# Optimization experiments

Hardware: AMD Instinct MI355X
Metric: run time of the kernel (lower is better)

Reference implementation:

```python
import jax, jax.numpy as jnp
import numpy as np
import math


def setup_inputs() -> dict:
    key = jax.random.key(0)
    k_fm, k_x, k_y, k_w, k_h = jax.random.split(key, 5)
    C, H, W = 512, 256, 256
    N = 4096
    patch_num = 4
    pe = 2  # sqrt(patch_num)
    feature_map = jax.random.normal(k_fm, (C, H, W), dtype=jnp.float32)
    # Boxes fully inside the map with per-patch extent >= 2 so every sub-box is valid.
    min_wh = 2.0 * pe + 1.0
    x0 = jax.random.uniform(k_x, (N,), minval=0.0, maxval=W / 2 - 1.0)
    y0 = jax.random.uniform(k_y, (N,), minval=0.0, maxval=H / 2 - 1.0)
    w = jax.random.uniform(k_w, (N,), minval=min_wh, maxval=W / 2 - 2.0)
    h = jax.random.uniform(k_h, (N,), minval=min_wh, maxval=H / 2 - 2.0)
    roi_batch = jnp.stack([x0, y0, x0 + w, y0 + h], axis=1).astype(jnp.float32)
    return {"feature_map": feature_map, "roi_batch": roi_batch, "patch_num": patch_num}


def _box_indices(roi_batch, patch_num, W):
    """Rounded, clamped per-patch sub-box corners; shapes (P, N), flattened patch-major."""
    pe = int(math.isqrt(patch_num))
    xmin, ymin, xmax, ymax = (roi_batch[:, k] for k in range(4))
    i = jnp.arange(patch_num)
    ix = (i % pe).astype(roi_batch.dtype)[:, None]
    iy = (i // pe).astype(roi_batch.dtype)[:, None]
    ws = ((xmax - xmin) / pe)[None, :]
    hs = ((ymax - ymin) / pe)[None, :]
    ax = xmin[None, :] + ix * ws  # (P, N)
    ay = ymin[None, :] + iy * hs
    clampi = lambda v: jnp.clip(jnp.round(v), 0, W - 1).astype(jnp.int32)
    x0, x1 = clampi(ax), clampi(ax + ws)
    y0, y1 = clampi(ay), clampi(ay + hs)
    flat = lambda a: a.reshape(-1)  # loop order: patch outer, roi inner
    return flat(x0), flat(x1), flat(y0), flat(y1)


def reference(feature_map, roi_batch, patch_num):
    C, H, W = feature_map.shape
    x0, x1, y0, y1 = _box_indices(roi_batch, patch_num, W)
    cw = x1 - x0
    ch = y1 - y0
    mask = (cw >= 1) & (ch >= 1)  # (P*N,)
    # Integral image with zero row/col padding: S[:, y, x] = sum of fm[:, :y, :x]
    S = jnp.pad(jnp.cumsum(jnp.cumsum(feature_map, axis=1), axis=2),
                ((0, 0), (1, 0), (1, 0)))
    # Region sums via 4-corner gather: (C, B)
    sums = S[:, y1, x1] - S[:, y0, x1] - S[:, y1, x0] + S[:, y0, x0]
    area = jnp.maximum(cw * ch, 1).astype(feature_map.dtype)
    pooled = (sums / area).T  # (B, C) region means == adaptive_avg_pool2d(.,(1,1))
    pooled = pooled * mask.astype(feature_map.dtype)[:, None]
    return pooled[:, :, None, None], mask.astype(jnp.int32)
```

## Files before the change

kernel.cpp:

```cpp
#include <hip/hip_runtime.h>


#define CHN 512
#define HD  256
#define WD  256
#define SP  257
#define YC  8
#define NK  32
#define OP_OFF 33817088UL

#define BAR() do { asm volatile("s_waitcnt lgkmcnt(0)" ::: "memory"); \
                   __builtin_amdgcn_s_barrier(); \
                   asm volatile("" ::: "memory"); } while (0)

__global__ __launch_bounds__(512, 4) void fusedScanK(const float* __restrict__ fm,
                                                     float* __restrict__ S) {
    __shared__ float tile[2][32][260];
    const int t = threadIdx.x, lane = t & 63, w = t >> 6;
    const int c0 = blockIdx.x * 32;
    const int k  = blockIdx.y;
    const int y0 = k * YC;

    const int cg = t & 7;
    const int x8 = t >> 3;
    const float4 z4 = make_float4(0.f, 0.f, 0.f, 0.f);

    if (k == 0) {
        #pragma unroll
        for (int it = 0; it < 4; ++it) {
            const int lin = it * 512 + t;
            const int cgg = lin & 7, x = lin >> 3;
            *(float4*)(S + (size_t)x * CHN + c0 + 4 * cgg) = z4;
        }
    }

    float4 cur[4], nxt[4];
    #pragma unroll
    for (int j = 0; j < 4; ++j)
        cur[j] = *(const float4*)(fm + ((size_t)(c0 + w * 4 + j) << 16)
                                     + (size_t)y0 * 256 + 4 * lane);

    float4 acc[4];
    #pragma unroll
    for (int m = 0; m < 4; ++m) acc[m] = z4;

    const int wcol = (4 * lane) ^ (4 * w);
    const int rxor = 4 * cg;

    for (int y = 0; y < YC; ++y) {
        const int buf = y & 1;
        if (y < YC - 1) {
            #pragma unroll
            for (int j = 0; j < 4; ++j)
                nxt[j] = *(const float4*)(fm + ((size_t)(c0 + w * 4 + j) << 16)
                                             + (size_t)(y0 + y + 1) * 256 + 4 * lane);
        }
        #pragma unroll
        for (int j = 0; j < 4; ++j) {
            const float4 v = cur[j];
            const float local = ((v.x + v.y) + v.z) + v.w;
            float s = local;
            #pragma unroll
            for (int d = 1; d < 64; d <<= 1) {
                float u = __shfl_up(s, d, 64);
                if (lane >= d) s += u;
            }
            const float e = s - local;
            float4 p;
            p.x = e   + v.x;
            p.y = p.x + v.y;
            p.z = p.y + v.z;
            p.w = p.z + v.w;
            *(float4*)&tile[buf][w * 4 + j][wcol] = p;
        }
        BAR();
        const size_t rowb = ((size_t)(y0 + y + 1) * SP) * CHN;
        #pragma unroll
        for (int m = 0; m < 4; ++m) {
            const int x = x8 + 64 * m;
            const int xs = x ^ rxor;
            float4 a = acc[m];
            a.x += tile[buf][4 * cg + 0][xs];
            a.y += tile[buf][4 * cg + 1][xs];
            a.z += tile[buf][4 * cg + 2][xs];
            a.w += tile[buf][4 * cg + 3][xs];
            acc[m] = a;
            *(float4*)(S + rowb + (size_t)(x + 1) * CHN + c0 + 4 * cg) = a;
        }
        if (t < 8)
            *(float4*)(S + rowb + c0 + 4 * t) = z4;
        #pragma unroll
        for (int j = 0; j < 4; ++j) cur[j] = nxt[j];
    }
}

__global__ __launch_bounds__(256) void offsetK(const float* __restrict__ S,
                                               float* __restrict__ OP) {
    const int gid = blockIdx.x * 256 + threadIdx.x;
    const int c = gid & 511, x = gid >> 9;
    OP[((size_t)0 * SP + x) * CHN + c] = 0.0f;
    OP[((size_t)1 * SP + x) * CHN + c] = 0.0f;
    double run = 0.0;
    #pragma unroll
    for (int j = 0; j < NK - 1; ++j) {
        run += (double)S[((size_t)(YC * (j + 1)) * SP + x) * CHN + c];
        OP[((size_t)(j + 2) * SP + x) * CHN + c] = (float)run;
    }
}

__global__ __launch_bounds__(256) void gatherK(const float* __restrict__ S,
                                              const float* __restrict__ OP,
                                              const float* __restrict__ roi,
                                              float* __restrict__ out,
                                              float* __restrict__ maskOut,
                                              int N) {
    const int n = blockIdx.x;
    const float xmin = roi[4 * n + 0];
    const float ymin = roi[4 * n + 1];
    const float xmax = roi[4 * n + 2];
    const float ymax = roi[4 * n + 3];

    const float wsv = __fdiv_rn(__fsub_rn(xmax, xmin), 2.0f);
    const float hsv = __fdiv_rn(__fsub_rn(ymax, ymin), 2.0f);
    const float ax1 = __fadd_rn(xmin, wsv);
    const float ay1 = __fadd_rn(ymin, hsv);
    const float lim = (float)(WD - 1);

    int rx[3], ry[3];
    rx[0] = (int)fminf(fmaxf(rintf(xmin), 0.0f), lim);
    rx[1] = (int)fminf(fmaxf(rintf(ax1), 0.0f), lim);
    rx[2] = (int)fminf(fmaxf(rintf(__fadd_rn(ax1, wsv)), 0.0f), lim);
    ry[0] = (int)fminf(fmaxf(rintf(ymin), 0.0f), lim);
    ry[1] = (int)fminf(fmaxf(rintf(ay1), 0.0f), lim);
    ry[2] = (int)fminf(fmaxf(rintf(__fadd_rn(ay1, hsv)), 0.0f), lim);

    const int t = threadIdx.x;
    float2 g[3][3];
    #pragma unroll
    for (int j = 0; j < 3; ++j) {
        const int kk = (ry[j] + YC - 1) >> 3;
        #pragma unroll
        for (int i = 0; i < 3; ++i) {
            const float2 l = *(const float2*)(S  + ((size_t)ry[j] * SP + rx[i]) * CHN + 2 * t);
            const float2 o = *(const float2*)(OP + ((size_t)kk   * SP + rx[i]) * CHN + 2 * t);
            g[j][i] = make_float2(l.x + o.x, l.y + o.y);
        }
    }

    float m[4];
    #pragma unroll
    for (int p = 0; p < 4; ++p) {
        const int ix = p & 1, iy = p >> 1;
        const int cw = rx[ix + 1] - rx[ix];
        const int ch = ry[iy + 1] - ry[iy];
        const int maskv = (cw >= 1 && ch >= 1) ? 1 : 0;
        int areai = cw * ch; if (areai < 1) areai = 1;
        const float areaf = (float)areai;
        const float maskf = (float)maskv;
        m[p] = maskf;

        const float2 s11 = g[iy + 1][ix + 1];
        const float2 s01 = g[iy][ix + 1];
        const float2 s10 = g[iy + 1][ix];
        const float2 s00 = g[iy][ix];
        float2 o;
        o.x = __fdiv_rn(((s11.x - s01.x) - s10.x) + s00.x, areaf) * maskf;
        o.y = __fdiv_rn(((s11.y - s01.y) - s10.y) + s00.y, areaf) * maskf;
        *(float2*)(out + ((size_t)p * N + n) * CHN + 2 * t) = o;
    }
    if (t < 4) maskOut[(size_t)t * N + n] = m[t];
}

extern "C" void kernel_launch(void* const* d_in, const int* in_sizes, int n_in,
                              void* d_out, int out_size, void* d_ws, size_t ws_size,
                              hipStream_t stream) {
    const float* fm  = (const float*)d_in[0];
    const float* roi = (const float*)d_in[1];

    const int N = in_sizes[1] / 4;
    const int B = 4 * N;

    float* S  = (float*)d_ws;
    float* OP = (float*)d_ws + OP_OFF;
    float* out     = (float*)d_out;
    float* maskOut = out + (size_t)B * CHN;

    dim3 gF(CHN / 32, NK);
    fusedScanK<<<gF, 512, 0, stream>>>(fm, S);

    offsetK<<<(SP * CHN) / 256, 256, 0, stream>>>(S, OP);

    gatherK<<<N, 256, 0, stream>>>(S, OP, roi, out, maskOut, N);
}
```

Baseline: 266.8 us.

## Re-layout integral image into channel-block-major tiles of 32 channels

Changes the summed-area table and the per-block offset table from a [y][x][512-channel] layout to [channel-block][y][x][32], and updates all three kernels to match. Each scan block now writes one contiguous region per row instead of 128-byte pieces spread with a 2 KB stride, which should improve write locality. The cost is that each gather block now reads 16 separate 128-byte segments at far-apart addresses per corner, instead of one contiguous 2 KB span. The offset kernel also has to use a div/mod to recover its indices.

```diff
diff --git a/kernel.cpp b/kernel.cpp
--- a/kernel.cpp
+++ b/kernel.cpp
@@ -9,6 +9,9 @@
 #define NK  32
 #define OP_OFF 33817088UL
 
+#define SIDX(cb, y, x)  ((((size_t)(cb) * SP + (y)) * SP + (x)) * 32)
+#define OPIDX(cb, kk, x) ((((size_t)(cb) * 33 + (kk)) * SP + (x)) * 32)
+
 #define BAR() do { asm volatile("s_waitcnt lgkmcnt(0)" ::: "memory"); \
                    __builtin_amdgcn_s_barrier(); \
                    asm volatile("" ::: "memory"); } while (0)
@@ -17,7 +20,8 @@
                                                      float* __restrict__ S) {
     __shared__ float tile[2][32][260];
     const int t = threadIdx.x, lane = t & 63, w = t >> 6;
-    const int c0 = blockIdx.x * 32;
+    const int cb = blockIdx.x;
+    const int c0 = cb * 32;
     const int k  = blockIdx.y;
     const int y0 = k * YC;
 
@@ -30,7 +34,7 @@
         for (int it = 0; it < 4; ++it) {
             const int lin = it * 512 + t;
             const int cgg = lin & 7, x = lin >> 3;
-            *(float4*)(S + (size_t)x * CHN + c0 + 4 * cgg) = z4;
+            *(float4*)(S + SIDX(cb, 0, x) + 4 * cgg) = z4;
         }
     }
 
@@ -74,7 +78,7 @@
             *(float4*)&tile[buf][w * 4 + j][wcol] = p;
         }
         BAR();
-        const size_t rowb = ((size_t)(y0 + y + 1) * SP) * CHN;
+        const size_t rowb = SIDX(cb, y0 + y + 1, 0);
         #pragma unroll
         for (int m = 0; m < 4; ++m) {
             const int x = x8 + 64 * m;
@@ -85,10 +89,10 @@
             a.z += tile[buf][4 * cg + 2][xs];
             a.w += tile[buf][4 * cg + 3][xs];
             acc[m] = a;
-            *(float4*)(S + rowb + (size_t)(x + 1) * CHN + c0 + 4 * cg) = a;
+            *(float4*)(S + rowb + (size_t)(x + 1) * 32 + 4 * cg) = a;
         }
         if (t < 8)
-            *(float4*)(S + rowb + c0 + 4 * t) = z4;
+            *(float4*)(S + rowb + 4 * t) = z4;
         #pragma unroll
         for (int j = 0; j < 4; ++j) cur[j] = nxt[j];
     }
@@ -97,14 +101,17 @@
 __global__ __launch_bounds__(256) void offsetK(const float* __restrict__ S,
                                                float* __restrict__ OP) {
     const int gid = blockIdx.x * 256 + threadIdx.x;
-    const int c = gid & 511, x = gid >> 9;
-    OP[((size_t)0 * SP + x) * CHN + c] = 0.0f;
-    OP[((size_t)1 * SP + x) * CHN + c] = 0.0f;
+    const int cc = gid & 31;
+    const int xr = gid >> 5;
+    const int x  = xr % SP;
+    const int cb = xr / SP;
+    OP[OPIDX(cb, 0, x) + cc] = 0.0f;
+    OP[OPIDX(cb, 1, x) + cc] = 0.0f;
     double run = 0.0;
     #pragma unroll
     for (int j = 0; j < NK - 1; ++j) {
-        run += (double)S[((size_t)(YC * (j + 1)) * SP + x) * CHN + c];
-        OP[((size_t)(j + 2) * SP + x) * CHN + c] = (float)run;
+        run += (double)S[SIDX(cb, YC * (j + 1), x) + cc];
+        OP[OPIDX(cb, j + 2, x) + cc] = (float)run;
     }
 }
 
@@ -135,14 +142,16 @@
     ry[2] = (int)fminf(fmaxf(rintf(__fadd_rn(ay1, hsv)), 0.0f), lim);
 
     const int t = threadIdx.x;
+    const int cbb = t >> 4;
+    const int cc  = (t & 15) * 2;
     float2 g[3][3];
     #pragma unroll
     for (int j = 0; j < 3; ++j) {
         const int kk = (ry[j] + YC - 1) >> 3;
         #pragma unroll
         for (int i = 0; i < 3; ++i) {
-            const float2 l = *(const float2*)(S  + ((size_t)ry[j] * SP + rx[i]) * CHN + 2 * t);
-            const float2 o = *(const float2*)(OP + ((size_t)kk   * SP + rx[i]) * CHN + 2 * t);
+            const float2 l = *(const float2*)(S  + SIDX(cbb, ry[j], rx[i]) + cc);
+            const float2 o = *(const float2*)(OP + OPIDX(cbb, kk, rx[i]) + cc);
             g[j][i] = make_float2(l.x + o.x, l.y + o.y);
         }
     }
@@ -185,10 +194,10 @@
     float* out     = (float*)d_out;
     float* maskOut = out + (size_t)B * CHN;
 
-    dim3 gF(CHN / 32, NK);
+    dim3 gF(16, NK);
     fusedScanK<<<gF, 512, 0, stream>>>(fm, S);
 
-    offsetK<<<(SP * CHN) / 256, 256, 0, stream>>>(S, OP);
+    offsetK<<<(16 * SP * 32) / 256, 256, 0, stream>>>(S, OP);
 
     gatherK<<<N, 256, 0, stream>>>(S, OP, roi, out, maskOut, N);
 }
```

After: 265.1 us. About the same (-0.6%).
